# Kernel tuning notes

Hardware: AMD Instinct MI355X
Metric: run time of the kernel (lower is better)

Reference implementation:

```python
import jax, jax.numpy as jnp
import numpy as np

H, NH, HD, KV, GS, L, F, V = 2048, 32, 64, 8, 4, 4, 8192, 32000
ROPE_BASE = 500000.0
EPS = 1e-5
WSCALE = 0.02


def setup_inputs() -> dict:
    key = jax.random.key(0)
    ks = jax.random.split(key, 12)
    B, S = 1, 2048
    return {
        "input_ids": jax.random.randint(ks[0], (B, S), 0, V),
        "embed": jax.random.normal(ks[1], (V, H), jnp.float32) * WSCALE,
        "ln1": jnp.ones((L, H), jnp.float32),
        "Wq": jax.random.normal(ks[2], (L, H, H), jnp.float32) * WSCALE,
        "Wk": jax.random.normal(ks[3], (L, KV * HD, H), jnp.float32) * WSCALE,
        "Wv": jax.random.normal(ks[4], (L, KV * HD, H), jnp.float32) * WSCALE,
        "Wo": jax.random.normal(ks[5], (L, H, H), jnp.float32) * WSCALE,
        "ln2": jnp.ones((L, H), jnp.float32),
        "Wg": jax.random.normal(ks[6], (L, F, H), jnp.float32) * WSCALE,
        "Wu": jax.random.normal(ks[7], (L, F, H), jnp.float32) * WSCALE,
        "Wd": jax.random.normal(ks[8], (L, H, F), jnp.float32) * WSCALE,
        "final_ln": jnp.ones((H,), jnp.float32),
    }


def _rms_norm(x, w):
    return x * jax.lax.rsqrt(jnp.mean(x * x, axis=-1, keepdims=True) + EPS) * w


def reference(input_ids, embed, ln1, Wq, Wk, Wv, Wo, ln2, Wg, Wu, Wd, final_ln):
    B, S = input_ids.shape
    h = embed[input_ids]                                   # [B,S,H]

    # RoPE tables (position_offset=0, prompt phase)
    dim_half = HD // 2
    inv_freq = 1.0 / (ROPE_BASE ** (jnp.arange(dim_half, dtype=jnp.float32) / dim_half))
    ang = jnp.arange(S, dtype=jnp.float32)[:, None] * inv_freq  # [S,dim_half]
    sin = jnp.sin(ang)[None, :, None, :]
    cos = jnp.cos(ang)[None, :, None, :]

    def rope(x):  # x: [B,S,heads,HD], halves layout as in source
        xe, xo = x[..., :dim_half], x[..., dim_half:2 * dim_half]
        return jnp.concatenate([xe * cos - xo * sin, xo * cos + xe * sin], axis=-1)

    causal = jnp.triu(jnp.ones((S, S), bool), k=1)          # [S,S]
    scale = 1.0 / (HD ** 0.5)

    for i in range(L):
        hn = _rms_norm(h, ln1[i])
        q = (hn @ Wq[i].T).reshape(B, S, NH, HD)
        k = (hn @ Wk[i].T).reshape(B, S, KV, HD)
        v = (hn @ Wv[i].T).reshape(B, S, KV, HD)
        q, k = rope(q), rope(k)
        ke = jnp.repeat(k, GS, axis=2)                      # GQA expand -> [B,S,NH,HD]
        ve = jnp.repeat(v, GS, axis=2)
        scores = jnp.einsum('bqhd,bkhd->bhqk', q, ke) * scale
        scores = jnp.where(causal[None, None], -jnp.inf, scores)
        attn = jax.nn.softmax(scores, axis=-1)
        out = jnp.einsum('bhqk,bkhd->bqhd', attn, ve).reshape(B, S, H)
        h = h + out @ Wo[i].T
        hn = _rms_norm(h, ln2[i])
        h = h + (jax.nn.silu(hn @ Wg[i].T) * (hn @ Wu[i].T)) @ Wd[i].T

    h = _rms_norm(h, final_ln)
    logits = h @ embed.T                                    # tied lm_head
    return logits
```

## Files before the change

### kernel.cpp

```cpp
#include <hip/hip_runtime.h>
#include <math.h>

#define HDIM 2048
#define SEQ 2048
#define NHEADS 32
#define KVH 8
#define HEADD 64
#define FDIM 8192
#define NLAYERS 4
#define VOCAB 32000

typedef __attribute__((ext_vector_type(4))) float f32x4;
typedef __attribute__((ext_vector_type(8))) short bf16x8;

__device__ __forceinline__ unsigned short f2b(float f) {
    unsigned int u = __float_as_uint(f);
    u += 0x7fff + ((u >> 16) & 1);
    return (unsigned short)(u >> 16);
}

__device__ __forceinline__ int xcd_swz(int bid, int nwg) {
    int xcd = bid & 7, lin = bid >> 3;
    int q = nwg >> 3, r = nwg & 7;
    return (xcd < r ? xcd * (q + 1) : r * (q + 1) + (xcd - r) * q) + lin;
}

#define GLL(gp, lp) __builtin_amdgcn_global_load_lds( \
    (const __attribute__((address_space(1))) void*)(gp), \
    (__attribute__((address_space(3))) void*)(lp), 16, 0, 0)

__device__ __forceinline__ void bar() {
    asm volatile("" ::: "memory");
    __builtin_amdgcn_s_barrier();
    asm volatile("" ::: "memory");
}

__global__ __launch_bounds__(256) void k_f2b(const float* __restrict__ src,
                                             unsigned short* __restrict__ dst, long n) {
    const long stride = (long)gridDim.x * 256 * 8;
    for (long i = ((long)blockIdx.x * 256 + threadIdx.x) * 8; i < n; i += stride) {
        float4 a = *(const float4*)(src + i);
        float4 b = *(const float4*)(src + i + 4);
        alignas(16) unsigned short t[8] = {f2b(a.x), f2b(a.y), f2b(a.z), f2b(a.w),
                                           f2b(b.x), f2b(b.y), f2b(b.z), f2b(b.w)};
        *(uint4*)(dst + i) = *(const uint4*)t;
    }
}

__global__ __launch_bounds__(256) void k_f2b_qkv(const float* __restrict__ Wq,
                                                 const float* __restrict__ Wk,
                                                 const float* __restrict__ Wv,
                                                 unsigned short* __restrict__ dst) {
    const long total = (long)NLAYERS * 3072 * 256;
    const long stride = (long)gridDim.x * 256;
    for (long u = (long)blockIdx.x * 256 + threadIdx.x; u < total; u += stride) {
        long l = u / (3072 * 256);
        long rem = u - l * (3072 * 256);
        long row = rem >> 8, cv = rem & 255;
        const float* src;
        if (row < 2048)      src = Wq + ((l * 2048 + row) << 11) + (cv << 3);
        else if (row < 2560) src = Wk + ((l * 512 + row - 2048) << 11) + (cv << 3);
        else                 src = Wv + ((l * 512 + row - 2560) << 11) + (cv << 3);
        float4 a = *(const float4*)src;
        float4 b = *(const float4*)(src + 4);
        alignas(16) unsigned short t[8] = {f2b(a.x), f2b(a.y), f2b(a.z), f2b(a.w),
                                           f2b(b.x), f2b(b.y), f2b(b.z), f2b(b.w)};
        *(uint4*)(dst + (u << 3)) = *(const uint4*)t;
    }
}

__global__ __launch_bounds__(256) void k_f2b_gu(const float* __restrict__ Wg,
                                                const float* __restrict__ Wu,
                                                unsigned short* __restrict__ dst) {
    const long total = (long)NLAYERS * 16384 * 256;
    const long stride = (long)gridDim.x * 256;
    for (long u = (long)blockIdx.x * 256 + threadIdx.x; u < total; u += stride) {
        long l = u / (16384 * 256);
        long rem = u - l * (16384 * 256);
        long row = rem >> 8, cv = rem & 255;
        long f = row >> 1;
        const float* src = ((row & 1) ? Wu : Wg) + ((l * FDIM + f) << 11) + (cv << 3);
        float4 a = *(const float4*)src;
        float4 b = *(const float4*)(src + 4);
        alignas(16) unsigned short t[8] = {f2b(a.x), f2b(a.y), f2b(a.z), f2b(a.w),
                                           f2b(b.x), f2b(b.y), f2b(b.z), f2b(b.w)};
        *(uint4*)(dst + (u << 3)) = *(const uint4*)t;
    }
}

template <int MODE, int K, int LDA, int LDB>
__global__ __launch_bounds__(512) void k_gemm256(const unsigned short* __restrict__ A,
                                                 const unsigned short* __restrict__ B,
                                                 float* __restrict__ C,
                                                 unsigned short* __restrict__ Cg,
                                                 int ldc, int mtiles, int nt,
                                                 long cstride) {
    constexpr int nK = K / 64;
    static_assert(nK >= 4 && (nK & 1) == 0, "nK must be even >= 4");
    __shared__ unsigned short As[2][2][128 * 64];
    __shared__ unsigned short Bs[2][2][128 * 64];
    const int tid  = threadIdx.x;
    const int lane = tid & 63;
    const int w    = tid >> 6;
    const int wm   = w >> 2, wn = w & 3;
    const int swz  = xcd_swz(blockIdx.x, gridDim.x);
    const int kslice = swz / nt;
    const int tile   = swz - kslice * nt;
    const int bm   = (tile % mtiles) * 256, bn = (tile / mtiles) * 256;
    const int r16  = lane & 15;
    const int l4   = lane >> 4;
    const int sw   = r16 & 7;

    const int srow = lane >> 3;
    const int scol = ((lane & 7) ^ srow) * 8;
    const unsigned short* Abase = A + (size_t)kslice * K
                                + (size_t)(bm + w * 16 + srow) * LDA + scol;
    const unsigned short* Bbase = B + (size_t)kslice * K
                                + (size_t)(bn + w * 16 + srow) * LDB + scol;

#define STG_A(bb, hh, kk) do { \
    GLL(Abase + (size_t)(hh) * 128 * LDA + (kk),       &As[(bb)][(hh)][(w * 16) * 64]); \
    GLL(Abase + (size_t)((hh) * 128 + 8) * LDA + (kk), &As[(bb)][(hh)][(w * 16 + 8) * 64]); \
} while (0)
#define STG_B(bb, hh, kk) do { \
    GLL(Bbase + (size_t)(hh) * 128 * LDB + (kk),       &Bs[(bb)][(hh)][(w * 16) * 64]); \
    GLL(Bbase + (size_t)((hh) * 128 + 8) * LDB + (kk), &Bs[(bb)][(hh)][(w * 16 + 8) * 64]); \
} while (0)

    f32x4 acc[8][4] = {};
    const int cb0 = ((0 + l4) ^ sw) * 8;
    const int cb1 = ((4 + l4) ^ sw) * 8;

    STG_A(0, 0, 0); STG_A(0, 1, 0); STG_B(0, 0, 0); STG_B(0, 1, 0);
    STG_B(1, 0, 64); STG_B(1, 1, 64); STG_A(1, 0, 64);
    asm volatile("s_waitcnt vmcnt(6)" ::: "memory");
    bar();

#define BLOAD(b) do { \
    const unsigned short* _Bh = Bs[b][wn >> 1]; \
    _Pragma("unroll") \
    for (int _n = 0; _n < 4; _n++) { \
        bq[_n][0] = *(const bf16x8*)&_Bh[((wn & 1) * 64 + _n * 16 + r16) * 64 + cb0]; \
        bq[_n][1] = *(const bf16x8*)&_Bh[((wn & 1) * 64 + _n * 16 + r16) * 64 + cb1]; \
    } \
} while (0)

#define PHASE(b, p, EXTRA, TAIL) do { \
    constexpr int _m0 = 2 * (p), _m1 = _m0 + 1; \
    const unsigned short* _Ah = As[b][_m0 >> 2]; \
    bf16x8 _a00 = *(const bf16x8*)&_Ah[(wm * 16 + (_m0 & 3) * 32 + r16) * 64 + cb0]; \
    bf16x8 _a01 = *(const bf16x8*)&_Ah[(wm * 16 + (_m0 & 3) * 32 + r16) * 64 + cb1]; \
    bf16x8 _a10 = *(const bf16x8*)&_Ah[(wm * 16 + (_m1 & 3) * 32 + r16) * 64 + cb0]; \
    bf16x8 _a11 = *(const bf16x8*)&_Ah[(wm * 16 + (_m1 & 3) * 32 + r16) * 64 + cb1]; \
    EXTRA; \
    bar(); \
    asm volatile("s_waitcnt lgkmcnt(0)" ::: "memory"); \
    __builtin_amdgcn_s_setprio(1); \
    _Pragma("unroll") \
    for (int _n = 0; _n < 4; _n++) { \
        acc[_m0][_n] = __builtin_amdgcn_mfma_f32_16x16x32_bf16(_a00, bq[_n][0], acc[_m0][_n], 0, 0, 0); \
        acc[_m0][_n] = __builtin_amdgcn_mfma_f32_16x16x32_bf16(_a01, bq[_n][1], acc[_m0][_n], 0, 0, 0); \
    } \
    _Pragma("unroll") \
    for (int _n = 0; _n < 4; _n++) { \
        acc[_m1][_n] = __builtin_amdgcn_mfma_f32_16x16x32_bf16(_a10, bq[_n][0], acc[_m1][_n], 0, 0, 0); \
        acc[_m1][_n] = __builtin_amdgcn_mfma_f32_16x16x32_bf16(_a11, bq[_n][1], acc[_m1][_n], 0, 0, 0); \
    } \
    __builtin_amdgcn_s_setprio(0); \
    TAIL; \
    bar(); \
} while (0)

#define TILE_STEADY(b, t) do { \
    bf16x8 bq[4][2]; \
    PHASE(b, 0, { BLOAD(b); STG_A((b) ^ 1, 1, ((t) + 1) * 64); }, ); \
    PHASE(b, 1, STG_B(b, 0, ((t) + 2) * 64), ); \
    PHASE(b, 2, STG_B(b, 1, ((t) + 2) * 64), ); \
    PHASE(b, 3, STG_A(b, 0, ((t) + 2) * 64), \
          asm volatile("s_waitcnt vmcnt(6)" ::: "memory")); \
} while (0)

#define TILE_2NDLAST(b, t) do { \
    bf16x8 bq[4][2]; \
    PHASE(b, 0, { BLOAD(b); STG_A((b) ^ 1, 1, ((t) + 1) * 64); }, ); \
    PHASE(b, 1, , ); \
    PHASE(b, 2, , ); \
    PHASE(b, 3, , asm volatile("s_waitcnt vmcnt(0)" ::: "memory")); \
} while (0)

#define TILE_LAST(b) do { \
    bf16x8 bq[4][2]; \
    PHASE(b, 0, BLOAD(b), ); \
    PHASE(b, 1, , ); \
    PHASE(b, 2, , ); \
    PHASE(b, 3, , ); \
} while (0)

    for (int t = 0; t < nK - 2; t += 2) {
        TILE_STEADY(0, t);
        TILE_STEADY(1, t + 1);
    }
    TILE_2NDLAST(0, nK - 2);
    TILE_LAST(1);

#undef TILE_STEADY
#undef TILE_2NDLAST
#undef TILE_LAST
#undef PHASE
#undef BLOAD
#undef STG_A
#undef STG_B

    if (MODE == 0) C += (size_t)kslice * cstride;
    const int r0 = l4 * 4;
#pragma unroll
    for (int m = 0; m < 8; m++)
#pragma unroll
        for (int n = 0; n < 4; n++)
#pragma unroll
            for (int j = 0; j < 4; j++) {
                int row = bm + wm * 16 + m * 32 + r0 + j;
                int col = bn + wn * 64 + n * 16 + r16;
                if (MODE == 0) {
                    C[(size_t)row * ldc + col] = acc[m][n][j];
                } else {
                    float v0 = acc[m][n][j];
                    float v1 = __shfl_xor(v0, 1, 64);
                    if (!(r16 & 1)) {
                        float val = v0 / (1.f + __expf(-v0)) * v1;
                        Cg[(size_t)row * ldc + (col >> 1)] = f2b(val);
                    }
                }
            }
}

__device__ __forceinline__ float rms_scale(float4 a, float4 b, int tid) {
    float sum = a.x*a.x + a.y*a.y + a.z*a.z + a.w*a.w
              + b.x*b.x + b.y*b.y + b.z*b.z + b.w*b.w;
#pragma unroll
    for (int off = 32; off; off >>= 1) sum += __shfl_xor(sum, off, 64);
    __shared__ float red[4];
    if ((tid & 63) == 0) red[tid >> 6] = sum;
    __syncthreads();
    float tot = red[0] + red[1] + red[2] + red[3];
    return rsqrtf(tot * (1.0f / HDIM) + 1e-5f);
}

__global__ __launch_bounds__(256) void k_rms_radd(unsigned short* __restrict__ out,
                                                  float* __restrict__ h,
                                                  const float* __restrict__ P, long n,
                                                  const float* __restrict__ w) {
    const int s = blockIdx.x, tid = threadIdx.x;
    const size_t base = (size_t)s * HDIM + tid * 8;
    float4 a = *(const float4*)(h + base);
    float4 b = *(const float4*)(h + base + 4);
#pragma unroll
    for (int k = 0; k < 4; k++) {
        const float* p = P + (size_t)k * n + base;
        float4 x = *(const float4*)p;
        float4 y = *(const float4*)(p + 4);
        a.x += x.x; a.y += x.y; a.z += x.z; a.w += x.w;
        b.x += y.x; b.y += y.y; b.z += y.z; b.w += y.w;
    }
    *(float4*)(h + base) = a;
    *(float4*)(h + base + 4) = b;
    float r = rms_scale(a, b, tid);
    const float4* wv = (const float4*)w;
    float4 wa = wv[tid*2], wb = wv[tid*2+1];
    alignas(16) unsigned short t[8];
    t[0] = f2b(a.x*r*wa.x); t[1] = f2b(a.y*r*wa.y);
    t[2] = f2b(a.z*r*wa.z); t[3] = f2b(a.w*r*wa.w);
    t[4] = f2b(b.x*r*wb.x); t[5] = f2b(b.y*r*wb.y);
    t[6] = f2b(b.z*r*wb.z); t[7] = f2b(b.w*r*wb.w);
    *(uint4*)(out + base) = *(const uint4*)t;
}

__global__ __launch_bounds__(256) void k_rmsnorm_bf(unsigned short* __restrict__ out,
                                                    const float* __restrict__ in,
                                                    const float* __restrict__ w) {
    const int s = blockIdx.x, tid = threadIdx.x;
    const float4* x = (const float4*)(in + (size_t)s * HDIM);
    float4 a = x[tid*2], b = x[tid*2+1];
    float r = rms_scale(a, b, tid);
    const float4* wv = (const float4*)w;
    float4 wa = wv[tid*2], wb = wv[tid*2+1];
    alignas(16) unsigned short t[8];
    t[0] = f2b(a.x*r*wa.x); t[1] = f2b(a.y*r*wa.y);
    t[2] = f2b(a.z*r*wa.z); t[3] = f2b(a.w*r*wa.w);
    t[4] = f2b(b.x*r*wb.x); t[5] = f2b(b.y*r*wb.y);
    t[6] = f2b(b.z*r*wb.z); t[7] = f2b(b.w*r*wb.w);
    *(uint4*)(out + (size_t)s * HDIM + tid * 8) = *(const uint4*)t;
}

__global__ __launch_bounds__(256) void k_rmsnorm_f32(float* __restrict__ out,
                                                     const float* __restrict__ in,
                                                     const float* __restrict__ w) {
    const int s = blockIdx.x, tid = threadIdx.x;
    const float4* x = (const float4*)(in + (size_t)s * HDIM);
    float4 a = x[tid*2], b = x[tid*2+1];
    float r = rms_scale(a, b, tid);
    const float4* wv = (const float4*)w;
    float4 wa = wv[tid*2], wb = wv[tid*2+1];
    float4* o = (float4*)(out + (size_t)s * HDIM);
    float4 oa, ob;
    oa.x = a.x*r*wa.x; oa.y = a.y*r*wa.y; oa.z = a.z*r*wa.z; oa.w = a.w*r*wa.w;
    ob.x = b.x*r*wb.x; ob.y = b.y*r*wb.y; ob.z = b.z*r*wb.z; ob.w = b.w*r*wb.w;
    o[tid*2] = oa; o[tid*2+1] = ob;
}

template <bool ACCUM>
__global__ __launch_bounds__(256) void k_gemm_bf(const unsigned short* __restrict__ A,
                                                 const unsigned short* __restrict__ B,
                                                 float* __restrict__ C,
                                                 int K, int lda, int ldb, int ldc,
                                                 int mtiles) {
    __shared__ unsigned short As[128 * 32];
    __shared__ unsigned short Bs[128 * 32];
    const int tid  = threadIdx.x;
    const int lane = tid & 63;
    const int w    = tid >> 6;
    const int wm   = w >> 1, wn = w & 1;
    const int bid  = xcd_swz(blockIdx.x, gridDim.x);
    const int bm   = (bid % mtiles) * 128, bn = (bid / mtiles) * 128;
    const int r16  = lane & 15;
    const int l4   = lane >> 4;

    const unsigned short* Ag = A + (size_t)(bm + w * 32 + (lane >> 2)) * lda + (lane & 3) * 8;
    const unsigned short* Bg = B + (size_t)(bn + w * 32 + (lane >> 2)) * ldb + (lane & 3) * 8;
    unsigned short* Al = As + w * 1024;
    unsigned short* Bl = Bs + w * 1024;

    f32x4 acc[4][4] = {};

    for (int k0 = 0; k0 < K; k0 += 32) {
        GLL(Ag + k0,                    Al);
        GLL(Ag + k0 + (size_t)16 * lda, Al + 512);
        GLL(Bg + k0,                    Bl);
        GLL(Bg + k0 + (size_t)16 * ldb, Bl + 512);
        __syncthreads();

        bf16x8 af[4], bf[4];
#pragma unroll
        for (int m = 0; m < 4; m++) af[m] = *(const bf16x8*)&As[(wm * 64 + m * 16 + r16) * 32 + l4 * 8];
#pragma unroll
        for (int n = 0; n < 4; n++) bf[n] = *(const bf16x8*)&Bs[(wn * 64 + n * 16 + r16) * 32 + l4 * 8];
#pragma unroll
        for (int m = 0; m < 4; m++)
#pragma unroll
            for (int n = 0; n < 4; n++)
                acc[m][n] = __builtin_amdgcn_mfma_f32_16x16x32_bf16(af[m], bf[n], acc[m][n], 0, 0, 0);
        __syncthreads();
    }

    const int r0 = l4 * 4;
#pragma unroll
    for (int m = 0; m < 4; m++)
#pragma unroll
        for (int n = 0; n < 4; n++)
#pragma unroll
            for (int j = 0; j < 4; j++) {
                int row = bm + wm * 64 + m * 16 + r0 + j;
                int col = bn + wn * 64 + n * 16 + r16;
                size_t idx = (size_t)row * ldc + col;
                if (ACCUM) C[idx] += acc[m][n][j];
                else       C[idx] = acc[m][n][j];
            }
}

template <bool ACCUM>
__global__ __launch_bounds__(256) void k_gemm(const float* __restrict__ A,
                                              const float* __restrict__ B,
                                              float* __restrict__ C,
                                              int K, int lda, int ldb, int ldc) {
    __shared__ unsigned short As[128][40];
    __shared__ unsigned short Bs[128][40];
    const int tid  = threadIdx.x;
    const int lane = tid & 63;
    const int wid  = tid >> 6;
    const int wm   = wid >> 1, wn = wid & 1;
    const int bm   = blockIdx.y * 128, bn = blockIdx.x * 128;
    const int arow = tid >> 1, ahalf = tid & 1;
    const float* Ab = A + (size_t)(bm + arow) * lda + ahalf * 16;
    const float* Bb = B + (size_t)(bn + arow) * ldb + ahalf * 16;
    const int r16 = lane & 15;
    const int kk  = (lane >> 4) * 8;

    f32x4 acc[4][4] = {};

    for (int k0 = 0; k0 < K; k0 += 32) {
        alignas(16) unsigned short ta[16], tb[16];
#pragma unroll
        for (int i = 0; i < 4; i++) {
            float4 av = *(const float4*)(Ab + k0 + i * 4);
            float4 bv = *(const float4*)(Bb + k0 + i * 4);
            ta[i*4+0] = f2b(av.x); ta[i*4+1] = f2b(av.y);
            ta[i*4+2] = f2b(av.z); ta[i*4+3] = f2b(av.w);
            tb[i*4+0] = f2b(bv.x); tb[i*4+1] = f2b(bv.y);
            tb[i*4+2] = f2b(bv.z); tb[i*4+3] = f2b(bv.w);
        }
        __syncthreads();
        *(uint4*)&As[arow][ahalf*16]     = *(const uint4*)&ta[0];
        *(uint4*)&As[arow][ahalf*16 + 8] = *(const uint4*)&ta[8];
        *(uint4*)&Bs[arow][ahalf*16]     = *(const uint4*)&tb[0];
        *(uint4*)&Bs[arow][ahalf*16 + 8] = *(const uint4*)&tb[8];
        __syncthreads();

        bf16x8 af[4], bf[4];
#pragma unroll
        for (int m = 0; m < 4; m++) af[m] = *(const bf16x8*)&As[wm*64 + m*16 + r16][kk];
#pragma unroll
        for (int n = 0; n < 4; n++) bf[n] = *(const bf16x8*)&Bs[wn*64 + n*16 + r16][kk];
#pragma unroll
        for (int m = 0; m < 4; m++)
#pragma unroll
            for (int n = 0; n < 4; n++)
                acc[m][n] = __builtin_amdgcn_mfma_f32_16x16x32_bf16(af[m], bf[n], acc[m][n], 0, 0, 0);
    }

    const int r0 = (lane >> 4) * 4;
#pragma unroll
    for (int m = 0; m < 4; m++)
#pragma unroll
        for (int n = 0; n < 4; n++)
#pragma unroll
            for (int j = 0; j < 4; j++) {
                int row = bm + wm*64 + m*16 + r0 + j;
                int col = bn + wn*64 + n*16 + r16;
                size_t idx = (size_t)row * ldc + col;
                if (ACCUM) C[idx] += acc[m][n][j];
                else       C[idx] = acc[m][n][j];
            }
}

__global__ __launch_bounds__(256) void k_gather(const int* __restrict__ ids,
                                                const float* __restrict__ embed,
                                                float* __restrict__ h) {
    const int s = blockIdx.x, tid = threadIdx.x;
    const int row = ids[s];
    const float4* src = (const float4*)(embed + (size_t)row * HDIM);
    float4* dst = (float4*)(h + (size_t)s * HDIM);
    dst[tid]       = src[tid];
    dst[tid + 256] = src[tid + 256];
}

template <bool TWO>
__global__ __launch_bounds__(256) void k_ropeq(const float* __restrict__ P0,
                                               const float* __restrict__ P1,
                                               unsigned short* __restrict__ q_bf) {
    const int s = blockIdx.x, tid = threadIdx.x;
    for (int idx = tid; idx < 1024; idx += 256) {
        int hh = idx >> 5, j = idx & 31;
        float invf = exp2f(-(float)j * (18.931568569324174f / 32.0f));
        float ang = (float)s * invf;
        float sn, cs;
        __sincosf(ang, &sn, &cs);
        size_t off = (size_t)s * 3072 + hh * 64 + j;
        float xe = P0[off]      + (TWO ? P1[off]      : 0.f);
        float xo = P0[off + 32] + (TWO ? P1[off + 32] : 0.f);
        unsigned short* o = q_bf + (size_t)s * HDIM + hh * 64 + j;
        o[0]  = f2b((xe * cs - xo * sn) * 0.125f);
        o[32] = f2b((xo * cs + xe * sn) * 0.125f);
    }
}

template <bool TWO>
__global__ __launch_bounds__(256) void k_prep_kv(const float* __restrict__ P0,
                                                 const float* __restrict__ P1,
                                                 unsigned short* __restrict__ kbf,
                                                 unsigned short* __restrict__ vtb) {
    const int s0 = blockIdx.x * 64, tid = threadIdx.x;
    for (int i = tid; i < 64 * 256; i += 256) {
        int r = i >> 8, idx = i & 255;
        int kvh = idx >> 5, j = idx & 31;
        int s = s0 + r;
        float invf = exp2f(-(float)j * (18.931568569324174f / 32.0f));
        float ang = (float)s * invf;
        float sn, cs;
        __sincosf(ang, &sn, &cs);
        size_t off = (size_t)s * 3072 + 2048 + kvh * 64 + j;
        float xe = P0[off]      + (TWO ? P1[off]      : 0.f);
        float xo = P0[off + 32] + (TWO ? P1[off + 32] : 0.f);
        unsigned short* o = kbf + ((size_t)kvh * SEQ + s) * 64;
        const int sw8 = s & 7;
        const int c1 = j + 32;
        o[((((j  >> 3)) ^ sw8) << 3) | (j  & 7)] = f2b(xe * cs - xo * sn);
        o[((((c1 >> 3)) ^ sw8) << 3) | (c1 & 7)] = f2b(xo * cs + xe * sn);
    }
    __shared__ float Ls[64][65];
    for (int kvh = 0; kvh < KVH; kvh++) {
        __syncthreads();
        {
            int r = tid >> 2, c0 = (tid & 3) * 16;
            size_t off = (size_t)(s0 + r) * 3072 + 2560 + kvh * 64 + c0;
#pragma unroll
            for (int i = 0; i < 16; i += 4) {
                float4 x = *(const float4*)(P0 + off + i);
                if (TWO) {
                    float4 y = *(const float4*)(P1 + off + i);
                    x.x += y.x; x.y += y.y; x.z += y.z; x.w += y.w;
                }
                Ls[r][c0+i] = x.x; Ls[r][c0+i+1] = x.y;
                Ls[r][c0+i+2] = x.z; Ls[r][c0+i+3] = x.w;
            }
        }
        __syncthreads();
        {
            int d = tid >> 2, k0 = (tid & 3) * 16;
            alignas(16) unsigned short tmp[16];
#pragma unroll
            for (int i = 0; i < 16; i++) tmp[i] = f2b(Ls[k0 + i][d]);
            unsigned short* dst = vtb + ((size_t)kvh * 64 + d) * SEQ + s0;
            const int b0 = k0 >> 3, dw = d & 7;
            *(uint4*)(dst + (((b0    ) ^ dw) << 3)) = *(const uint4*)tmp;
            *(uint4*)(dst + (((b0 + 1) ^ dw) << 3)) = *(const uint4*)(tmp + 8);
        }
    }
}

__global__ __launch_bounds__(256) void k_attn2(const unsigned short* __restrict__ q_bf,
                                               const unsigned short* __restrict__ kbf,
                                               const unsigned short* __restrict__ vtb,
                                               unsigned short* __restrict__ aob) {
    const int hh  = blockIdx.y;
    const int qt  = gridDim.x - 1 - blockIdx.x;
    const int qb  = qt * 64;
    const int kvh = hh >> 2;
    const int tid = threadIdx.x, w = tid >> 6, lane = tid & 63;
    const int r16 = lane & 15;
    const int l4  = lane >> 4;
    const int sw  = r16 & 7;
    const int cb0 = ((0 + l4) ^ sw) * 8;
    const int cb1 = ((4 + l4) ^ sw) * 8;

    __shared__ unsigned short Ks[2][64 * 64];
    __shared__ unsigned short Vs[2][64 * 64];
    __shared__ unsigned short Ps[64][72];

    bf16x8 qf[2];
    {
        const unsigned short* qrow = q_bf + (size_t)(qb + w*16 + r16) * HDIM + hh * 64;
        qf[0] = *(const bf16x8*)(qrow + l4 * 8);
        qf[1] = *(const bf16x8*)(qrow + 32 + l4 * 8);
    }

    float l[4] = {0.f, 0.f, 0.f, 0.f};
    f32x4 out[4] = {};
    const int ntiles = qt + 1;

    for (int t0 = 0; t0 < ntiles; t0 += 2) {
        const bool two = (t0 + 1 < ntiles);
        __syncthreads();
        {
            const unsigned short* ksrc = kbf + ((size_t)kvh * SEQ + t0 * 64 + w * 16) * 64
                                       + (size_t)lane * 8;
            GLL(ksrc,       &Ks[0][(w * 16) * 64]);
            GLL(ksrc + 512, &Ks[0][(w * 16 + 8) * 64]);
            const unsigned short* vsrc = vtb
                + ((size_t)(kvh * 64 + w * 16 + (lane >> 3))) * SEQ
                + t0 * 64 + (lane & 7) * 8;
            GLL(vsrc,           &Vs[0][(w * 16) * 64]);
            GLL(vsrc + 8 * SEQ, &Vs[0][(w * 16 + 8) * 64]);
            if (two) {
                GLL(ksrc + 4096,       &Ks[1][(w * 16) * 64]);
                GLL(ksrc + 4096 + 512, &Ks[1][(w * 16 + 8) * 64]);
                GLL(vsrc + 64,           &Vs[1][(w * 16) * 64]);
                GLL(vsrc + 64 + 8 * SEQ, &Vs[1][(w * 16 + 8) * 64]);
            }
        }
        __syncthreads();

        f32x4 s[2][4] = {};
#pragma unroll
        for (int n = 0; n < 4; n++) {
            bf16x8 kf0 = *(const bf16x8*)&Ks[0][(n*16 + r16) * 64 + cb0];
            bf16x8 kf1 = *(const bf16x8*)&Ks[0][(n*16 + r16) * 64 + cb1];
            s[0][n] = __builtin_amdgcn_mfma_f32_16x16x32_bf16(qf[0], kf0, s[0][n], 0, 0, 0);
            s[0][n] = __builtin_amdgcn_mfma_f32_16x16x32_bf16(qf[1], kf1, s[0][n], 0, 0, 0);
        }
        if (two) {
#pragma unroll
            for (int n = 0; n < 4; n++) {
                bf16x8 kf0 = *(const bf16x8*)&Ks[1][(n*16 + r16) * 64 + cb0];
                bf16x8 kf1 = *(const bf16x8*)&Ks[1][(n*16 + r16) * 64 + cb1];
                s[1][n] = __builtin_amdgcn_mfma_f32_16x16x32_bf16(qf[0], kf0, s[1][n], 0, 0, 0);
                s[1][n] = __builtin_amdgcn_mfma_f32_16x16x32_bf16(qf[1], kf1, s[1][n], 0, 0, 0);
            }
        }

        const int dh = qt - t0;
        if (dh < 2) {
#pragma unroll
            for (int n = 0; n < 4; n++)
#pragma unroll
                for (int j = 0; j < 4; j++) {
                    int qrow = w*16 + l4*4 + j;
                    int key  = n*16 + r16;
                    if (key > qrow) { if (dh == 0) s[0][n][j] = -1e30f; else s[1][n][j] = -1e30f; }
                }
        }

#pragma unroll
        for (int j = 0; j < 4; j++) {
            float rp = 0.f;
#pragma unroll
            for (int n = 0; n < 4; n++) {
                float p = __expf(s[0][n][j]);
                s[0][n][j] = p;
                rp += p;
            }
            if (two) {
#pragma unroll
                for (int n = 0; n < 4; n++) {
                    float p = __expf(s[1][n][j]);
                    s[1][n][j] = p;
                    rp += p;
                }
            }
            l[j] += rp;
        }

#pragma unroll
        for (int n = 0; n < 4; n++)
#pragma unroll
            for (int j = 0; j < 4; j++)
                Ps[w*16 + l4*4 + j][n*16 + r16] = f2b(s[0][n][j]);
#pragma unroll
        for (int ks = 0; ks < 2; ks++) {
            bf16x8 pa = *(const bf16x8*)&Ps[w*16 + r16][ks*32 + l4*8];
            const int cb = ks ? cb1 : cb0;
#pragma unroll
            for (int n = 0; n < 4; n++) {
                bf16x8 vf = *(const bf16x8*)&Vs[0][(n*16 + r16) * 64 + cb];
                out[n] = __builtin_amdgcn_mfma_f32_16x16x32_bf16(pa, vf, out[n], 0, 0, 0);
            }
        }
        if (two) {
#pragma unroll
            for (int n = 0; n < 4; n++)
#pragma unroll
                for (int j = 0; j < 4; j++)
                    Ps[w*16 + l4*4 + j][n*16 + r16] = f2b(s[1][n][j]);
#pragma unroll
            for (int ks = 0; ks < 2; ks++) {
                bf16x8 pa = *(const bf16x8*)&Ps[w*16 + r16][ks*32 + l4*8];
                const int cb = ks ? cb1 : cb0;
#pragma unroll
                for (int n = 0; n < 4; n++) {
                    bf16x8 vf = *(const bf16x8*)&Vs[1][(n*16 + r16) * 64 + cb];
                    out[n] = __builtin_amdgcn_mfma_f32_16x16x32_bf16(pa, vf, out[n], 0, 0, 0);
                }
            }
        }
    }

#pragma unroll
    for (int j = 0; j < 4; j++) {
#pragma unroll
        for (int off = 1; off < 16; off <<= 1) l[j] += __shfl_xor(l[j], off, 64);
    }

#pragma unroll
    for (int n = 0; n < 4; n++)
#pragma unroll
        for (int j = 0; j < 4; j++) {
            int row = qb + w*16 + l4*4 + j;
            int col = hh*64 + n*16 + r16;
            aob[(size_t)row * HDIM + col] = f2b(out[n][j] / l[j]);
        }
}

__global__ __launch_bounds__(256) void k_rope(float* __restrict__ x, int nh,
                                              float scale, int ld) {
    const int s = blockIdx.x, tid = threadIdx.x;
    const int total = nh * 32;
    for (int idx = tid; idx < total; idx += 256) {
        int hh = idx >> 5, j = idx & 31;
        float invf = exp2f(-(float)j * (18.931568569324174f / 32.0f));
        float ang = (float)s * invf;
        float sn, cs;
        __sincosf(ang, &sn, &cs);
        float* p = x + (size_t)s * ld + hh * 64 + j;
        float xe = p[0], xo = p[32];
        p[0]  = (xe * cs - xo * sn) * scale;
        p[32] = (xo * cs + xe * sn) * scale;
    }
}

__global__ __launch_bounds__(256) void k_vtrans(const float* __restrict__ v, int ldv,
                                                unsigned short* __restrict__ vt) {
    __shared__ float Ls[64][65];
    const int tid = threadIdx.x;
    const int kb = blockIdx.x * 64, db = blockIdx.y * 64;
    {
        int r = tid >> 2, c0 = (tid & 3) * 16;
        const float* src = v + (size_t)(kb + r) * ldv + db + c0;
#pragma unroll
        for (int i = 0; i < 16; i += 4) {
            float4 x = *(const float4*)(src + i);
            Ls[r][c0+i] = x.x; Ls[r][c0+i+1] = x.y;
            Ls[r][c0+i+2] = x.z; Ls[r][c0+i+3] = x.w;
        }
    }
    __syncthreads();
    {
        int d = tid >> 2, k0 = (tid & 3) * 16;
        alignas(16) unsigned short tmp[16];
#pragma unroll
        for (int i = 0; i < 16; i++) tmp[i] = f2b(Ls[k0 + i][d]);
        unsigned short* dst = vt + (size_t)(db + d) * SEQ + kb + k0;
        *(uint4*)dst       = *(const uint4*)tmp;
        *(uint4*)(dst + 8) = *(const uint4*)(tmp + 8);
    }
}

__global__ __launch_bounds__(256) void k_attn_f32(float* __restrict__ q, int ldq,
                                                  const float* __restrict__ kb, int ldk,
                                                  const unsigned short* __restrict__ vt) {
    const int hh  = blockIdx.y;
    const int qt  = gridDim.x - 1 - blockIdx.x;
    const int qb  = qt * 64;
    const int kvh = hh >> 2;
    const int tid = threadIdx.x, w = tid >> 6, lane = tid & 63;
    const int r16 = lane & 15;
    const int l4  = lane >> 4;

    __shared__ unsigned short Ks[64][72];
    __shared__ unsigned short Vs[64][72];
    __shared__ unsigned short Ps[64][72];

    bf16x8 qf[2];
    {
        const float* qrow = q + (size_t)(qb + w*16 + r16) * ldq + hh * 64;
#pragma unroll
        for (int ks = 0; ks < 2; ks++) {
            alignas(16) unsigned short t[8];
#pragma unroll
            for (int i = 0; i < 8; i += 4) {
                float4 x = *(const float4*)(qrow + ks*32 + l4*8 + i);
                t[i] = f2b(x.x); t[i+1] = f2b(x.y); t[i+2] = f2b(x.z); t[i+3] = f2b(x.w);
            }
            qf[ks] = *(const bf16x8*)t;
        }
    }

    float m[4] = {-1e30f, -1e30f, -1e30f, -1e30f};
    float l[4] = {0.f, 0.f, 0.f, 0.f};
    f32x4 out[4] = {};

    for (int t = 0; t <= qt; t++) {
        __syncthreads();
        {
            int r = tid >> 2, c0 = (tid & 3) * 16;
            const float* src = kb + (size_t)(t*64 + r) * ldk + kvh*64 + c0;
            alignas(16) unsigned short tmp[16];
#pragma unroll
            for (int i = 0; i < 16; i += 4) {
                float4 x = *(const float4*)(src + i);
                tmp[i]   = f2b(x.x); tmp[i+1] = f2b(x.y);
                tmp[i+2] = f2b(x.z); tmp[i+3] = f2b(x.w);
            }
            *(uint4*)&Ks[r][c0]     = *(const uint4*)tmp;
            *(uint4*)&Ks[r][c0 + 8] = *(const uint4*)(tmp + 8);
            const unsigned short* vsrc = vt + (size_t)(kvh*64 + r) * SEQ + t*64 + c0;
            *(uint4*)&Vs[r][c0]     = *(const uint4*)vsrc;
            *(uint4*)&Vs[r][c0 + 8] = *(const uint4*)(vsrc + 8);
        }
        __syncthreads();

        f32x4 s[4] = {};
#pragma unroll
        for (int ks = 0; ks < 2; ks++)
#pragma unroll
            for (int n = 0; n < 4; n++) {
                bf16x8 kf = *(const bf16x8*)&Ks[n*16 + r16][ks*32 + l4*8];
                s[n] = __builtin_amdgcn_mfma_f32_16x16x32_bf16(qf[ks], kf, s[n], 0, 0, 0);
            }

        if (t == qt) {
#pragma unroll
            for (int n = 0; n < 4; n++)
#pragma unroll
                for (int j = 0; j < 4; j++) {
                    int qrow = w*16 + l4*4 + j;
                    int key  = n*16 + r16;
                    if (key > qrow) s[n][j] = -1e30f;
                }
        }

        float corr[4];
#pragma unroll
        for (int j = 0; j < 4; j++) {
            float mx = fmaxf(fmaxf(s[0][j], s[1][j]), fmaxf(s[2][j], s[3][j]));
#pragma unroll
            for (int off = 1; off < 16; off <<= 1) mx = fmaxf(mx, __shfl_xor(mx, off, 64));
            float mn = fmaxf(m[j], mx);
            corr[j] = __expf(m[j] - mn);
            m[j] = mn;
            float rs = 0.f;
#pragma unroll
            for (int n = 0; n < 4; n++) {
                float p = __expf(s[n][j] - mn);
                s[n][j] = p;
                rs += p;
            }
#pragma unroll
            for (int off = 1; off < 16; off <<= 1) rs += __shfl_xor(rs, off, 64);
            l[j] = l[j] * corr[j] + rs;
        }

#pragma unroll
        for (int n = 0; n < 4; n++)
#pragma unroll
            for (int j = 0; j < 4; j++)
                Ps[w*16 + l4*4 + j][n*16 + r16] = f2b(s[n][j]);

#pragma unroll
        for (int n = 0; n < 4; n++)
#pragma unroll
            for (int j = 0; j < 4; j++) out[n][j] *= corr[j];

#pragma unroll
        for (int ks = 0; ks < 2; ks++) {
            bf16x8 pa = *(const bf16x8*)&Ps[w*16 + r16][ks*32 + l4*8];
#pragma unroll
            for (int n = 0; n < 4; n++) {
                bf16x8 vf = *(const bf16x8*)&Vs[n*16 + r16][ks*32 + l4*8];
                out[n] = __builtin_amdgcn_mfma_f32_16x16x32_bf16(pa, vf, out[n], 0, 0, 0);
            }
        }
    }

#pragma unroll
    for (int n = 0; n < 4; n++)
#pragma unroll
        for (int j = 0; j < 4; j++)
            q[(size_t)(qb + w*16 + l4*4 + j) * ldq + hh*64 + n*16 + r16] = out[n][j] / l[j];
}

__global__ __launch_bounds__(256) void k_silu(float* __restrict__ g,
                                              const float* __restrict__ u) {
    const size_t i = (size_t)blockIdx.x * 256 + threadIdx.x;
    float4 gv = ((const float4*)g)[i];
    float4 uv = ((const float4*)u)[i];
    gv.x = gv.x / (1.f + __expf(-gv.x)) * uv.x;
    gv.y = gv.y / (1.f + __expf(-gv.y)) * uv.y;
    gv.z = gv.z / (1.f + __expf(-gv.z)) * uv.z;
    gv.w = gv.w / (1.f + __expf(-gv.w)) * uv.w;
    ((float4*)g)[i] = gv;
}

extern "C" void kernel_launch(void* const* d_in, const int* in_sizes, int n_in,
                              void* d_out, int out_size, void* d_ws, size_t ws_size,
                              hipStream_t stream) {
    (void)in_sizes; (void)n_in; (void)out_size;
    const int*   ids   = (const int*)d_in[0];
    const float* embed = (const float*)d_in[1];
    const float* ln1   = (const float*)d_in[2];
    const float* Wq    = (const float*)d_in[3];
    const float* Wk    = (const float*)d_in[4];
    const float* Wv    = (const float*)d_in[5];
    const float* Wo    = (const float*)d_in[6];
    const float* ln2   = (const float*)d_in[7];
    const float* Wg    = (const float*)d_in[8];
    const float* Wu    = (const float*)d_in[9];
    const float* Wd    = (const float*)d_in[10];
    const float* fln   = (const float*)d_in[11];
    float* out = (float*)d_out;

    char* base = (char*)d_ws;
    size_t off = 0;
    auto alloc = [&](size_t bytes) -> char* {
        char* r = base + off;
        off = (off + bytes + 255) & ~(size_t)255;
        return r;
    };
    float* h     = (float*)alloc((size_t)SEQ * HDIM * 4);
    unsigned short* hn_bf = (unsigned short*)alloc((size_t)SEQ * HDIM * 2);
    unsigned short* aob   = (unsigned short*)alloc((size_t)SEQ * HDIM * 2);
    unsigned short* gated = (unsigned short*)alloc((size_t)SEQ * FDIM * 2);
    unsigned short* q_bf  = (unsigned short*)alloc((size_t)SEQ * HDIM * 2);
    unsigned short* kbf   = (unsigned short*)alloc((size_t)KVH * SEQ * 64 * 2);
    unsigned short* vtb   = (unsigned short*)alloc((size_t)KVH * 64 * SEQ * 2);
    unsigned short* wqkv  = (unsigned short*)alloc((size_t)NLAYERS * 3072 * HDIM * 2);
    unsigned short* wo_b  = (unsigned short*)alloc((size_t)NLAYERS * HDIM * HDIM * 2);
    unsigned short* wgu   = (unsigned short*)alloc((size_t)NLAYERS * 2 * FDIM * HDIM * 2);
    unsigned short* wd_b  = (unsigned short*)alloc((size_t)NLAYERS * HDIM * FDIM * 2);
    unsigned short* emb_b = (unsigned short*)alloc((size_t)VOCAB * HDIM * 2);
    char* Sreg = alloc((size_t)4 * SEQ * HDIM * 4);
    const size_t REQ_MAIN = off;
    const size_t REQ_FB2  = REQ_MAIN - (size_t)4 * SEQ * HDIM * 4
                          + (((size_t)SEQ * 3072 * 4 + 255) & ~(size_t)255);

    const long LQ = (long)HDIM * HDIM;
    const long LGU = 2L * FDIM * HDIM;
    const long LG = (long)FDIM * HDIM;
    const long MSZ = (long)SEQ * 3072;
    const long HSZ = (long)SEQ * HDIM;

    if (ws_size >= REQ_MAIN) {
        float* Pf = (float*)Sreg;
        k_f2b_qkv<<<2048, 256, 0, stream>>>(Wq, Wk, Wv, wqkv);
        k_f2b_gu<<<2048, 256, 0, stream>>>(Wg, Wu, wgu);
        k_f2b<<<2048, 256, 0, stream>>>(Wo, wo_b, (long)NLAYERS * LQ);
        k_f2b<<<2048, 256, 0, stream>>>(Wd, wd_b, (long)NLAYERS * LG);
        k_f2b<<<2048, 256, 0, stream>>>(embed, emb_b, (long)VOCAB * HDIM);

        k_gather<<<SEQ, 256, 0, stream>>>(ids, embed, h);
        k_rmsnorm_bf<<<SEQ, 256, 0, stream>>>(hn_bf, h, ln1);

        for (int i = 0; i < NLAYERS; i++) {
            k_gemm256<0, 1024, 2048, 2048><<<192, 512, 0, stream>>>(
                hn_bf, wqkv + (long)i * 3072 * HDIM, Pf, nullptr, 3072, 8, 96, MSZ);
            k_ropeq<true><<<SEQ, 256, 0, stream>>>(Pf, Pf + MSZ, q_bf);
            k_prep_kv<true><<<SEQ / 64, 256, 0, stream>>>(Pf, Pf + MSZ, kbf, vtb);
            k_attn2<<<dim3(SEQ / 64, NHEADS), 256, 0, stream>>>(q_bf, kbf, vtb, aob);
            k_gemm256<0, 512, 2048, 2048><<<256, 512, 0, stream>>>(
                aob, wo_b + (long)i * LQ, Pf, nullptr, 2048, 8, 64, HSZ);
            k_rms_radd<<<SEQ, 256, 0, stream>>>(hn_bf, h, Pf, HSZ, ln2 + i * HDIM);
            k_gemm256<2, 2048, 2048, 2048><<<512, 512, 0, stream>>>(
                hn_bf, wgu + (long)i * LGU, nullptr, gated, FDIM, 8, 512, 0);
            k_gemm256<0, 2048, 8192, 8192><<<256, 512, 0, stream>>>(
                gated, wd_b + (long)i * LG, Pf, nullptr, 2048, 8, 64, HSZ);
            const float* nw = (i + 1 < NLAYERS) ? ln1 + (i + 1) * HDIM : fln;
            k_rms_radd<<<SEQ, 256, 0, stream>>>(hn_bf, h, Pf, HSZ, nw);
        }

        k_gemm256<0, 2048, 2048, 2048><<<1000, 512, 0, stream>>>(
            hn_bf, emb_b, out, nullptr, VOCAB, 8, 1000, 0);
    } else if (ws_size >= REQ_FB2) {
        float* qkv = (float*)Sreg;
        k_f2b_qkv<<<2048, 256, 0, stream>>>(Wq, Wk, Wv, wqkv);
        k_f2b_gu<<<2048, 256, 0, stream>>>(Wg, Wu, wgu);
        k_f2b<<<2048, 256, 0, stream>>>(Wo, wo_b, (long)NLAYERS * LQ);
        k_f2b<<<2048, 256, 0, stream>>>(Wd, wd_b, (long)NLAYERS * LG);
        k_f2b<<<2048, 256, 0, stream>>>(embed, emb_b, (long)VOCAB * HDIM);

        k_gather<<<SEQ, 256, 0, stream>>>(ids, embed, h);

        for (int i = 0; i < NLAYERS; i++) {
            k_rmsnorm_bf<<<SEQ, 256, 0, stream>>>(hn_bf, h, ln1 + i * HDIM);
            k_gemm_bf<false><<<16 * 24, 256, 0, stream>>>(hn_bf, wqkv + (long)i*3072*HDIM,
                                                          qkv, HDIM, HDIM, HDIM, 3072, 16);
            k_ropeq<false><<<SEQ, 256, 0, stream>>>(qkv, nullptr, q_bf);
            k_prep_kv<false><<<SEQ / 64, 256, 0, stream>>>(qkv, nullptr, kbf, vtb);
            k_attn2<<<dim3(SEQ / 64, NHEADS), 256, 0, stream>>>(q_bf, kbf, vtb, aob);
            k_gemm_bf<true><<<16 * 16, 256, 0, stream>>>(aob, wo_b + (long)i*LQ, h,
                                                         HDIM, HDIM, HDIM, HDIM, 16);
            k_rmsnorm_bf<<<SEQ, 256, 0, stream>>>(hn_bf, h, ln2 + i * HDIM);
            k_gemm256<2, 2048, 2048, 2048><<<512, 512, 0, stream>>>(
                hn_bf, wgu + (long)i * LGU, nullptr, gated, FDIM, 8, 512, 0);
            k_gemm_bf<true><<<16 * 16, 256, 0, stream>>>(gated, wd_b + (long)i*LG, h,
                                                         FDIM, FDIM, FDIM, HDIM, 16);
        }

        k_rmsnorm_bf<<<SEQ, 256, 0, stream>>>(hn_bf, h, fln);
        k_gemm256<0, 2048, 2048, 2048><<<1000, 512, 0, stream>>>(
            hn_bf, emb_b, out, nullptr, VOCAB, 8, 1000, 0);
    } else {
        float* ws = (float*)d_ws;
        const size_t M4 = (size_t)4 * 1024 * 1024;
        const size_t M1 = (size_t)1 * 1024 * 1024;
        float* fh  = ws;
        float* hn  = fh + M4;
        float* q   = hn + M4;
        float* kb  = q  + M4;
        float* vb  = kb + M1;
        float* gb  = vb + M1;
        float* ub  = gb + M4;
        unsigned short* fvt = (unsigned short*)(ub + M4);

        k_gather<<<SEQ, 256, 0, stream>>>(ids, embed, fh);

        for (int i = 0; i < NLAYERS; i++) {
            const float* Wq_i = Wq + (size_t)i * HDIM * HDIM;
            const float* Wk_i = Wk + (size_t)i * 512 * HDIM;
            const float* Wv_i = Wv + (size_t)i * 512 * HDIM;
            const float* Wo_i = Wo + (size_t)i * HDIM * HDIM;
            const float* Wg_i = Wg + (size_t)i * FDIM * HDIM;
            const float* Wu_i = Wu + (size_t)i * FDIM * HDIM;
            const float* Wd_i = Wd + (size_t)i * HDIM * FDIM;

            k_rmsnorm_f32<<<SEQ, 256, 0, stream>>>(hn, fh, ln1 + i * HDIM);
            k_gemm<false><<<dim3(16, 16), 256, 0, stream>>>(hn, Wq_i, q,  HDIM, HDIM, HDIM, HDIM);
            k_gemm<false><<<dim3(4, 16),  256, 0, stream>>>(hn, Wk_i, kb, HDIM, HDIM, HDIM, 512);
            k_gemm<false><<<dim3(4, 16),  256, 0, stream>>>(hn, Wv_i, vb, HDIM, HDIM, HDIM, 512);
            k_rope<<<SEQ, 256, 0, stream>>>(q,  NHEADS, 0.125f, HDIM);
            k_rope<<<SEQ, 256, 0, stream>>>(kb, KVH,    1.0f,  512);
            k_vtrans<<<dim3(SEQ/64, 8), 256, 0, stream>>>(vb, 512, fvt);
            k_attn_f32<<<dim3(SEQ/64, NHEADS), 256, 0, stream>>>(q, HDIM, kb, 512, fvt);
            k_gemm<true><<<dim3(16, 16), 256, 0, stream>>>(q, Wo_i, fh, HDIM, HDIM, HDIM, HDIM);

            k_rmsnorm_f32<<<SEQ, 256, 0, stream>>>(hn, fh, ln2 + i * HDIM);
            for (int fc = 0; fc < 4; fc++) {
                const float* Wg_c = Wg_i + (size_t)fc * 2048 * HDIM;
                const float* Wu_c = Wu_i + (size_t)fc * 2048 * HDIM;
                const float* Wd_c = Wd_i + (size_t)fc * 2048;
                k_gemm<false><<<dim3(16, 16), 256, 0, stream>>>(hn, Wg_c, gb, HDIM, HDIM, HDIM, 2048);
                k_gemm<false><<<dim3(16, 16), 256, 0, stream>>>(hn, Wu_c, ub, HDIM, HDIM, HDIM, 2048);
                k_silu<<<4096, 256, 0, stream>>>(gb, ub);
                k_gemm<true><<<dim3(16, 16), 256, 0, stream>>>(gb, Wd_c, fh, 2048, 2048, FDIM, HDIM);
            }
        }

        k_rmsnorm_f32<<<SEQ, 256, 0, stream>>>(hn, fh, fln);
        k_gemm<false><<<dim3(VOCAB/128, 16), 256, 0, stream>>>(hn, embed, out, HDIM, HDIM, HDIM, VOCAB);
    }
}
```

Before: 2.255 ms.

## Software-pipeline A-fragment LDS reads one phase ahead of MFMAs in GEMM mainloop

Splits each GEMM phase into separate LDS-read and MFMA steps, using two register sets (x/y) so the A fragments for the next phase load while the current phase's MFMAs run. It removes the explicit lgkmcnt(0) wait that sat before each MFMA batch and reorders the MFMAs so the m0 and m1 accumulators interleave. Global-to-LDS staging is regrouped around the new barriers, and the per-tile barrier count drops from eight to five. The extra registers raise VGPR pressure. Correctness now depends on the compiler inserting the right LDS waits and on the reduced barriers still separating reads from overwrites.

Result: no change. 2.274 ms (+0.8%).

```diff
diff --git a/kernel.cpp b/kernel.cpp
--- a/kernel.cpp
+++ b/kernel.cpp
@@ -145,55 +145,89 @@
     } \
 } while (0)
 
-#define PHASE(b, p, EXTRA, TAIL) do { \
+#define AREAD(bb, p, d0, d1, d2, d3) do { \
     constexpr int _m0 = 2 * (p), _m1 = _m0 + 1; \
-    const unsigned short* _Ah = As[b][_m0 >> 2]; \
-    bf16x8 _a00 = *(const bf16x8*)&_Ah[(wm * 16 + (_m0 & 3) * 32 + r16) * 64 + cb0]; \
-    bf16x8 _a01 = *(const bf16x8*)&_Ah[(wm * 16 + (_m0 & 3) * 32 + r16) * 64 + cb1]; \
-    bf16x8 _a10 = *(const bf16x8*)&_Ah[(wm * 16 + (_m1 & 3) * 32 + r16) * 64 + cb0]; \
-    bf16x8 _a11 = *(const bf16x8*)&_Ah[(wm * 16 + (_m1 & 3) * 32 + r16) * 64 + cb1]; \
-    EXTRA; \
-    bar(); \
-    asm volatile("s_waitcnt lgkmcnt(0)" ::: "memory"); \
+    const unsigned short* _Ah = As[bb][_m0 >> 2]; \
+    d0 = *(const bf16x8*)&_Ah[(wm * 16 + (_m0 & 3) * 32 + r16) * 64 + cb0]; \
+    d1 = *(const bf16x8*)&_Ah[(wm * 16 + (_m0 & 3) * 32 + r16) * 64 + cb1]; \
+    d2 = *(const bf16x8*)&_Ah[(wm * 16 + (_m1 & 3) * 32 + r16) * 64 + cb0]; \
+    d3 = *(const bf16x8*)&_Ah[(wm * 16 + (_m1 & 3) * 32 + r16) * 64 + cb1]; \
+} while (0)
+
+#define MFMAP(p, s0, s1, s2, s3) do { \
+    constexpr int _m0 = 2 * (p), _m1 = _m0 + 1; \
     __builtin_amdgcn_s_setprio(1); \
     _Pragma("unroll") \
     for (int _n = 0; _n < 4; _n++) { \
-        acc[_m0][_n] = __builtin_amdgcn_mfma_f32_16x16x32_bf16(_a00, bq[_n][0], acc[_m0][_n], 0, 0, 0); \
-        acc[_m0][_n] = __builtin_amdgcn_mfma_f32_16x16x32_bf16(_a01, bq[_n][1], acc[_m0][_n], 0, 0, 0); \
+        acc[_m0][_n] = __builtin_amdgcn_mfma_f32_16x16x32_bf16(s0, bq[_n][0], acc[_m0][_n], 0, 0, 0); \
+        acc[_m1][_n] = __builtin_amdgcn_mfma_f32_16x16x32_bf16(s2, bq[_n][0], acc[_m1][_n], 0, 0, 0); \
     } \
     _Pragma("unroll") \
     for (int _n = 0; _n < 4; _n++) { \
-        acc[_m1][_n] = __builtin_amdgcn_mfma_f32_16x16x32_bf16(_a10, bq[_n][0], acc[_m1][_n], 0, 0, 0); \
-        acc[_m1][_n] = __builtin_amdgcn_mfma_f32_16x16x32_bf16(_a11, bq[_n][1], acc[_m1][_n], 0, 0, 0); \
+        acc[_m0][_n] = __builtin_amdgcn_mfma_f32_16x16x32_bf16(s1, bq[_n][1], acc[_m0][_n], 0, 0, 0); \
+        acc[_m1][_n] = __builtin_amdgcn_mfma_f32_16x16x32_bf16(s3, bq[_n][1], acc[_m1][_n], 0, 0, 0); \
     } \
     __builtin_amdgcn_s_setprio(0); \
-    TAIL; \
-    bar(); \
 } while (0)
 
 #define TILE_STEADY(b, t) do { \
-    bf16x8 bq[4][2]; \
-    PHASE(b, 0, { BLOAD(b); STG_A((b) ^ 1, 1, ((t) + 1) * 64); }, ); \
-    PHASE(b, 1, STG_B(b, 0, ((t) + 2) * 64), ); \
-    PHASE(b, 2, STG_B(b, 1, ((t) + 2) * 64), ); \
-    PHASE(b, 3, STG_A(b, 0, ((t) + 2) * 64), \
-          asm volatile("s_waitcnt vmcnt(6)" ::: "memory")); \
+    bf16x8 bq[4][2], x0, x1, x2, x3, y0, y1, y2, y3; \
+    AREAD(b, 0, x0, x1, x2, x3); \
+    BLOAD(b); \
+    AREAD(b, 1, y0, y1, y2, y3); \
+    STG_A((b) ^ 1, 1, ((t) + 1) * 64); \
+    bar(); \
+    MFMAP(0, x0, x1, x2, x3); \
+    AREAD(b, 2, x0, x1, x2, x3); \
+    bar(); \
+    MFMAP(1, y0, y1, y2, y3); \
+    AREAD(b, 3, y0, y1, y2, y3); \
+    STG_B(b, 0, ((t) + 2) * 64); \
+    bar(); \
+    MFMAP(2, x0, x1, x2, x3); \
+    STG_B(b, 1, ((t) + 2) * 64); \
+    STG_A(b, 0, ((t) + 2) * 64); \
+    bar(); \
+    MFMAP(3, y0, y1, y2, y3); \
+    asm volatile("s_waitcnt vmcnt(6)" ::: "memory"); \
+    bar(); \
 } while (0)
 
 #define TILE_2NDLAST(b, t) do { \
-    bf16x8 bq[4][2]; \
-    PHASE(b, 0, { BLOAD(b); STG_A((b) ^ 1, 1, ((t) + 1) * 64); }, ); \
-    PHASE(b, 1, , ); \
-    PHASE(b, 2, , ); \
-    PHASE(b, 3, , asm volatile("s_waitcnt vmcnt(0)" ::: "memory")); \
+    bf16x8 bq[4][2], x0, x1, x2, x3, y0, y1, y2, y3; \
+    AREAD(b, 0, x0, x1, x2, x3); \
+    BLOAD(b); \
+    AREAD(b, 1, y0, y1, y2, y3); \
+    STG_A((b) ^ 1, 1, ((t) + 1) * 64); \
+    bar(); \
+    MFMAP(0, x0, x1, x2, x3); \
+    AREAD(b, 2, x0, x1, x2, x3); \
+    bar(); \
+    MFMAP(1, y0, y1, y2, y3); \
+    AREAD(b, 3, y0, y1, y2, y3); \
+    bar(); \
+    MFMAP(2, x0, x1, x2, x3); \
+    bar(); \
+    MFMAP(3, y0, y1, y2, y3); \
+    asm volatile("s_waitcnt vmcnt(0)" ::: "memory"); \
+    bar(); \
 } while (0)
 
 #define TILE_LAST(b) do { \
-    bf16x8 bq[4][2]; \
-    PHASE(b, 0, BLOAD(b), ); \
-    PHASE(b, 1, , ); \
-    PHASE(b, 2, , ); \
-    PHASE(b, 3, , ); \
+    bf16x8 bq[4][2], x0, x1, x2, x3, y0, y1, y2, y3; \
+    AREAD(b, 0, x0, x1, x2, x3); \
+    BLOAD(b); \
+    AREAD(b, 1, y0, y1, y2, y3); \
+    bar(); \
+    MFMAP(0, x0, x1, x2, x3); \
+    AREAD(b, 2, x0, x1, x2, x3); \
+    bar(); \
+    MFMAP(1, y0, y1, y2, y3); \
+    AREAD(b, 3, y0, y1, y2, y3); \
+    bar(); \
+    MFMAP(2, x0, x1, x2, x3); \
+    bar(); \
+    MFMAP(3, y0, y1, y2, y3); \
 } while (0)
 
     for (int t = 0; t < nK - 2; t += 2) {
@@ -206,7 +240,8 @@
 #undef TILE_STEADY
 #undef TILE_2NDLAST
 #undef TILE_LAST
-#undef PHASE
+#undef MFMAP
+#undef AREAD
 #undef BLOAD
 #undef STG_A
 #undef STG_B
```
